# Kernel tuning notes

Measured on AMD Instinct MI355X. Metric: run time of the kernel, lower is better.

The kernel has to match this reference:

```python
import jax, jax.numpy as jnp
import numpy as np

H = 96          # hidden_dim / GatedGraphConv out_channels
L = 6           # num_layers
F_IN = 32       # num_node_features
G = 4096        # number of graphs in batch
BN_EPS = 1e-5


def setup_inputs() -> dict:
    key = jax.random.key(0)
    ks = jax.random.split(key, 16)
    N, E = 100000, 400000
    x = jax.random.normal(ks[0], (N, F_IN), dtype=jnp.float32)
    edge_index = jax.random.randint(ks[1], (2, E), 0, N, dtype=jnp.int64)
    batch = jnp.sort(jax.random.randint(ks[2], (N,), 0, G, dtype=jnp.int64))
    s = 1.0 / np.sqrt(H)
    conv_w = jax.random.uniform(ks[3], (L, H, H), jnp.float32, -s, s)
    w_ih = jax.random.uniform(ks[4], (3 * H, H), jnp.float32, -s, s)
    w_hh = jax.random.uniform(ks[5], (3 * H, H), jnp.float32, -s, s)
    b_ih = jax.random.uniform(ks[6], (3 * H,), jnp.float32, -s, s)
    b_hh = jax.random.uniform(ks[7], (3 * H,), jnp.float32, -s, s)
    bn_gamma = jnp.ones((H,), jnp.float32)
    bn_beta = jnp.zeros((H,), jnp.float32)
    s1 = 1.0 / np.sqrt(H)
    fc1_w = jax.random.uniform(ks[8], (4 * H, H), jnp.float32, -s1, s1)
    fc1_b = jax.random.uniform(ks[9], (4 * H,), jnp.float32, -s1, s1)
    s2 = 1.0 / np.sqrt(4 * H)
    fc2_w = jax.random.uniform(ks[10], (H, 4 * H), jnp.float32, -s2, s2)
    fc2_b = jax.random.uniform(ks[11], (H,), jnp.float32, -s2, s2)
    fc3_w = jax.random.uniform(ks[12], (1, H), jnp.float32, -s1, s1)
    fc3_b = jax.random.uniform(ks[13], (1,), jnp.float32, -s1, s1)
    return dict(x=x, edge_index=edge_index, batch=batch, conv_w=conv_w,
                w_ih=w_ih, w_hh=w_hh, b_ih=b_ih, b_hh=b_hh,
                bn_gamma=bn_gamma, bn_beta=bn_beta,
                fc1_w=fc1_w, fc1_b=fc1_b, fc2_w=fc2_w, fc2_b=fc2_b,
                fc3_w=fc3_w, fc3_b=fc3_b)


def _gated_graph_conv(x, src, dst, conv_w, w_ih, w_hh, b_ih, b_hh):
    N = x.shape[0]
    # PyG zero-pads input features up to out_channels
    h = jnp.pad(x, ((0, 0), (0, H - x.shape[1])))
    for i in range(L):
        m = h @ conv_w[i]                         # [N, H]
        agg = jnp.zeros((N, H), m.dtype).at[dst].add(m[src])  # scatter-add at targets
        gi = agg @ w_ih.T + b_ih                  # [N, 3H]
        gh = h @ w_hh.T + b_hh                    # [N, 3H]
        i_r, i_z, i_n = jnp.split(gi, 3, axis=-1)
        h_r, h_z, h_n = jnp.split(gh, 3, axis=-1)
        r = jax.nn.sigmoid(i_r + h_r)
        z = jax.nn.sigmoid(i_z + h_z)
        n = jnp.tanh(i_n + r * h_n)
        h = (1.0 - z) * n + z * h
    return h


def reference(x, edge_index, batch, conv_w, w_ih, w_hh, b_ih, b_hh,
              bn_gamma, bn_beta, fc1_w, fc1_b, fc2_w, fc2_b, fc3_w, fc3_b):
    src, dst = edge_index[0], edge_index[1]
    h = _gated_graph_conv(x, src, dst, conv_w, w_ih, w_hh, b_ih, b_hh)
    h = jax.nn.relu(h)
    # global mean pool (dropout is identity in eval)
    sums = jax.ops.segment_sum(h, batch, num_segments=G)          # [G, H]
    counts = jax.ops.segment_sum(jnp.ones((h.shape[0],), h.dtype), batch, num_segments=G)
    pooled = sums / jnp.maximum(counts, 1.0)[:, None]
    # BatchNorm1d in eval mode: running_mean=0, running_var=1
    hbn = (pooled / jnp.sqrt(1.0 + BN_EPS)) * bn_gamma + bn_beta
    h1 = jax.nn.relu(hbn @ fc1_w.T + fc1_b)
    h2 = jax.nn.relu(h1 @ fc2_w.T + fc2_b)
    return h2 @ fc3_w.T + fc3_b                                    # [G, 1]
```

## Files before the change

### kernel.cpp

```cpp
#include <hip/hip_runtime.h>

#define H96 96
#define LAYERS 6
#define BN_EPS 1e-5f
#define SCAN_B 1024

typedef unsigned short u16;
typedef unsigned int u32;
typedef _Float16 f16;
typedef _Float16 h8 __attribute__((ext_vector_type(8)));
typedef float f32x4 __attribute__((ext_vector_type(4)));
typedef u32 u32x3 __attribute__((ext_vector_type(3)));

__device__ __forceinline__ float sigm(float x) { return 1.f / (1.f + __expf(-x)); }
__device__ __forceinline__ float tanh_(float x) { return 2.f / (1.f + __expf(-2.f * x)) - 1.f; }
__device__ __forceinline__ f32x4 splat4(float x) { f32x4 v = {x, x, x, x}; return v; }

struct h2s { f16 x, y; };

__device__ __forceinline__ void upk(u32 v, float& lo, float& hi) {
    union { u32 u; h2s h; } c;
    c.u = v;
    lo = (float)c.h.x;
    hi = (float)c.h.y;
}

__global__ void k_f2h(const float* __restrict__ convw, const float* __restrict__ wih,
                      const float* __restrict__ whh, const float* __restrict__ fc1w,
                      const float* __restrict__ fc2w, f16* __restrict__ dst) {
    int i = blockIdx.x * 256 + threadIdx.x;
    if (i >= 184320) return;
    float v;
    if (i < 55296) v = convw[i];
    else if (i < 82944) v = wih[i - 55296];
    else if (i < 110592) v = whh[i - 82944];
    else if (i < 147456) v = fc1w[i - 110592];
    else v = fc2w[i - 147456];
    dst[i] = (f16)v;
}

__global__ __launch_bounds__(256) void k_wpt(const f16* __restrict__ wih16, const f16* __restrict__ convw16,
                                             f16* __restrict__ wpt) {
    int l = blockIdx.y;
    int lane = threadIdx.x & 63, wave = threadIdx.x >> 6;
    int l15 = lane & 15, q = lane >> 4;
    int rowa = blockIdx.x * 64 + wave * 16 + l15;
    if (rowa >= 288) rowa = 287;
    const f16* B = convw16 + (size_t)l * 9216;
    h8 af[3];
#pragma unroll
    for (int s = 0; s < 3; s++) af[s] = *(const h8*)(wih16 + (size_t)rowa * 96 + s * 32 + q * 8);
    f32x4 acc[6];
#pragma unroll
    for (int t = 0; t < 6; t++) acc[t] = splat4(0.f);
#pragma unroll
    for (int s = 0; s < 3; s++)
#pragma unroll
        for (int t = 0; t < 6; t++) {
            h8 b = *(const h8*)(B + (size_t)(t * 16 + l15) * 96 + s * 32 + q * 8);
            acc[t] = __builtin_amdgcn_mfma_f32_16x16x32_f16(af[s], b, acc[t], 0, 0, 0);
        }
    int rbase = blockIdx.x * 64 + wave * 16 + q * 4;
#pragma unroll
    for (int t = 0; t < 6; t++)
#pragma unroll
        for (int rr = 0; rr < 4; rr++) {
            int row = rbase + rr;
            if (row < 288) wpt[(size_t)l * 27648 + (size_t)row * 96 + t * 16 + l15] = (f16)acc[t][rr];
        }
}

__global__ void k_pad(const float* __restrict__ x, f16* __restrict__ hf, int N) {
    int i = blockIdx.x * 256 + threadIdx.x;
    if (i >= N * H96) return;
    int n = i / H96, c = i - n * H96;
    float v = (c < 32) ? x[n * 32 + c] : 0.f;
    hf[i] = (f16)v;
}

__global__ void k_hist(const int* __restrict__ key, int* __restrict__ deg, int E) {
    int e = blockIdx.x * 256 + threadIdx.x;
    if (e < E) atomicAdd(&deg[key[e]], 1);
}

__global__ __launch_bounds__(SCAN_B) void k_scan1(const int* __restrict__ deg, int* __restrict__ incl,
                                                  int* __restrict__ bsum, int N) {
    __shared__ int sh[SCAN_B];
    int i = blockIdx.x * SCAN_B + threadIdx.x;
    int v = (i < N) ? deg[i] : 0;
    sh[threadIdx.x] = v;
    __syncthreads();
    for (int off = 1; off < SCAN_B; off <<= 1) {
        int t = (threadIdx.x >= (u32)off) ? sh[threadIdx.x - off] : 0;
        __syncthreads();
        sh[threadIdx.x] += t;
        __syncthreads();
    }
    incl[blockIdx.x * SCAN_B + threadIdx.x] = sh[threadIdx.x];
    if (threadIdx.x == SCAN_B - 1) bsum[blockIdx.x] = sh[threadIdx.x];
}

__global__ void k_scan2(int* __restrict__ bsum, int nb) {
    if (blockIdx.x == 0 && threadIdx.x == 0) {
        int run = 0;
        for (int i = 0; i < nb; i++) { run += bsum[i]; bsum[i] = run; }
    }
}

__global__ void k_scan3(const int* __restrict__ deg, const int* __restrict__ incl, const int* __restrict__ bsum,
                        int* __restrict__ rs, int* __restrict__ cur, int N, int E) {
    int i = blockIdx.x * 256 + threadIdx.x;
    if (i == 0) rs[N] = E;
    if (i < N) {
        int b = i / SCAN_B;
        int off = (b > 0) ? bsum[b - 1] : 0;
        int ex = incl[i] - deg[i] + off;
        rs[i] = ex;
        if (cur) cur[i] = ex;
    }
}

__global__ void k_fill(const int* __restrict__ src, const int* __restrict__ dst, int* __restrict__ cur,
                       int* __restrict__ es, int E) {
    int e = blockIdx.x * 256 + threadIdx.x;
    if (e < E) {
        int p = atomicAdd(&cur[dst[e]], 1);
        es[p] = src[e];
    }
}

__global__ __launch_bounds__(256) void k_gather(const f16* __restrict__ hin, const int* __restrict__ rs,
                                                const int* __restrict__ es, f16* __restrict__ agg, int N) {
    int grp = threadIdx.x >> 4;
    int lane6 = threadIdx.x & 15;
    int node = blockIdx.x * 16 + grp;
    if (node >= N) return;
    int s = rs[node], e = rs[node + 1];
    float a0 = 0, a1 = 0, a2 = 0, a3 = 0, a4 = 0, a5 = 0;
    const char* basep = (const char*)hin;
    int off = lane6 * 12;
    for (int i = s; i < e; i += 4) {
        int j1 = (i + 1 < e) ? i + 1 : i;
        int j2 = (i + 2 < e) ? i + 2 : i;
        int j3 = (i + 3 < e) ? i + 3 : i;
        float m1 = (i + 1 < e) ? 1.f : 0.f;
        float m2 = (i + 2 < e) ? 1.f : 0.f;
        float m3 = (i + 3 < e) ? 1.f : 0.f;
        int sa = es[i], sb = es[j1], sc = es[j2], sd = es[j3];
        u32x3 va = *(const u32x3*)(basep + (size_t)sa * 192 + off);
        u32x3 vb = *(const u32x3*)(basep + (size_t)sb * 192 + off);
        u32x3 vc = *(const u32x3*)(basep + (size_t)sc * 192 + off);
        u32x3 vd = *(const u32x3*)(basep + (size_t)sd * 192 + off);
        float t0, t1;
        upk(va.x, t0, t1); a0 += t0; a1 += t1;
        upk(va.y, t0, t1); a2 += t0; a3 += t1;
        upk(va.z, t0, t1); a4 += t0; a5 += t1;
        upk(vb.x, t0, t1); a0 += t0 * m1; a1 += t1 * m1;
        upk(vb.y, t0, t1); a2 += t0 * m1; a3 += t1 * m1;
        upk(vb.z, t0, t1); a4 += t0 * m1; a5 += t1 * m1;
        upk(vc.x, t0, t1); a0 += t0 * m2; a1 += t1 * m2;
        upk(vc.y, t0, t1); a2 += t0 * m2; a3 += t1 * m2;
        upk(vc.z, t0, t1); a4 += t0 * m2; a5 += t1 * m2;
        upk(vd.x, t0, t1); a0 += t0 * m3; a1 += t1 * m3;
        upk(vd.y, t0, t1); a2 += t0 * m3; a3 += t1 * m3;
        upk(vd.z, t0, t1); a4 += t0 * m3; a5 += t1 * m3;
    }
    f16* dp = agg + (size_t)node * H96 + lane6 * 6;
    h2s p0, p1, p2;
    p0.x = (f16)a0; p0.y = (f16)a1;
    p1.x = (f16)a2; p1.y = (f16)a3;
    p2.x = (f16)a4; p2.y = (f16)a5;
    *(h2s*)(dp + 0) = p0;
    *(h2s*)(dp + 2) = p1;
    *(h2s*)(dp + 4) = p2;
}

__global__ __launch_bounds__(384, 4) void k_gru(const f16* __restrict__ agg, const f16* __restrict__ hin,
                                                f16* __restrict__ hout, const f16* __restrict__ wpt,
                                                const f16* __restrict__ whh, const float* __restrict__ bih,
                                                const float* __restrict__ bhh, int N) {
    int w = threadIdx.x >> 6;
    int lane = threadIdx.x & 63;
    int l15 = lane & 15, q = lane >> 4;
    int jr = w * 16 + l15;
    float b_r = bih[jr] + bhh[jr];
    float b_z = bih[96 + jr] + bhh[96 + jr];
    float b_in = bih[192 + jr];
    float b_hn = bhh[192 + jr];
    h8 wr0[3], wr1[3], wz0[3], wz1[3], wn0[3], wn1[3];
#pragma unroll
    for (int s = 0; s < 3; s++) {
        int ko = s * 32 + q * 8;
        wr0[s] = *(const h8*)(wpt + (size_t)jr * H96 + ko);
        wz0[s] = *(const h8*)(wpt + (size_t)(96 + jr) * H96 + ko);
        wn0[s] = *(const h8*)(wpt + (size_t)(192 + jr) * H96 + ko);
        wr1[s] = *(const h8*)(whh + (size_t)jr * H96 + ko);
        wz1[s] = *(const h8*)(whh + (size_t)(96 + jr) * H96 + ko);
        wn1[s] = *(const h8*)(whh + (size_t)(192 + jr) * H96 + ko);
    }
    int ntiles = (N + 15) >> 4;
    for (int tile = blockIdx.x; tile < ntiles; tile += gridDim.x) {
        int base = tile << 4;
        int rowa = base + l15;
        if (rowa >= N) rowa = N - 1;
        h8 as_[3], ah[3];
#pragma unroll
        for (int s = 0; s < 3; s++) {
            as_[s] = *(const h8*)(agg + (size_t)rowa * H96 + s * 32 + q * 8);
            ah[s] = *(const h8*)(hin + (size_t)rowa * H96 + s * 32 + q * 8);
        }
        f32x4 r = splat4(b_r), z = splat4(b_z), nn = splat4(b_in), hn = splat4(b_hn);
#pragma unroll
        for (int s = 0; s < 3; s++) {
            r = __builtin_amdgcn_mfma_f32_16x16x32_f16(as_[s], wr0[s], r, 0, 0, 0);
            r = __builtin_amdgcn_mfma_f32_16x16x32_f16(ah[s], wr1[s], r, 0, 0, 0);
            z = __builtin_amdgcn_mfma_f32_16x16x32_f16(as_[s], wz0[s], z, 0, 0, 0);
            z = __builtin_amdgcn_mfma_f32_16x16x32_f16(ah[s], wz1[s], z, 0, 0, 0);
            nn = __builtin_amdgcn_mfma_f32_16x16x32_f16(as_[s], wn0[s], nn, 0, 0, 0);
            hn = __builtin_amdgcn_mfma_f32_16x16x32_f16(ah[s], wn1[s], hn, 0, 0, 0);
        }
        int rbase = base + q * 4;
#pragma unroll
        for (int rr = 0; rr < 4; rr++) {
            int row = rbase + rr;
            if (row < N) {
                float rv = sigm(r[rr]);
                float zv = sigm(z[rr]);
                float nv = tanh_(nn[rr] + rv * hn[rr]);
                size_t idx = (size_t)row * H96 + w * 16 + l15;
                float hold = (float)hin[idx];
                float hnew = (1.f - zv) * nv + zv * hold;
                hout[idx] = (f16)hnew;
            }
        }
    }
}

__global__ void k_pool2(const f16* __restrict__ hf, const int* __restrict__ grs,
                        const float* __restrict__ gamma, const float* __restrict__ beta,
                        f16* __restrict__ pooled, int Gn) {
    int g = blockIdx.x;
    int c = threadIdx.x;
    if (g >= Gn || c >= H96) return;
    int s = grs[g], e = grs[g + 1];
    float sum = 0.f;
    for (int n = s; n < e; n++) sum += fmaxf((float)hf[(size_t)n * H96 + c], 0.f);
    float cnt = fmaxf((float)(e - s), 1.f);
    float val = (sum / cnt) * (gamma[c] * rsqrtf(1.f + BN_EPS)) + beta[c];
    pooled[(size_t)g * H96 + c] = (f16)val;
}

template <int KS, int NT, int OUTW, bool RELU>
__global__ __launch_bounds__(256) void k_mlp(const f16* __restrict__ A, const f16* __restrict__ W,
                                             const float* __restrict__ bias, f16* __restrict__ out, int M) {
    int lane = threadIdx.x & 63, wave = threadIdx.x >> 6;
    int l15 = lane & 15, q = lane >> 4;
    int colBase = blockIdx.y * (NT * 16);
    int tile = blockIdx.x;
    int rowa = tile * 64 + wave * 16 + l15;
    if (rowa >= M) rowa = M - 1;
    h8 af[KS];
#pragma unroll
    for (int s = 0; s < KS; s++) af[s] = *(const h8*)(A + (size_t)rowa * (KS * 32) + s * 32 + q * 8);
    f32x4 acc[NT];
#pragma unroll
    for (int t = 0; t < NT; t++) acc[t] = splat4(0.f);
#pragma unroll
    for (int s = 0; s < KS; s++)
#pragma unroll
        for (int t = 0; t < NT; t++) {
            h8 b = *(const h8*)(W + (size_t)(colBase + t * 16 + l15) * (KS * 32) + s * 32 + q * 8);
            acc[t] = __builtin_amdgcn_mfma_f32_16x16x32_f16(af[s], b, acc[t], 0, 0, 0);
        }
    int rbase = tile * 64 + wave * 16 + q * 4;
#pragma unroll
    for (int t = 0; t < NT; t++) {
        float bv = bias[colBase + t * 16 + l15];
#pragma unroll
        for (int rr = 0; rr < 4; rr++) {
            int row = rbase + rr;
            if (row >= M) continue;
            float v = acc[t][rr] + bv;
            if (RELU) v = fmaxf(v, 0.f);
            out[(size_t)row * OUTW + colBase + t * 16 + l15] = (f16)v;
        }
    }
}

__global__ void k_mlp3(const f16* __restrict__ h2, const float* __restrict__ w, const float* __restrict__ b,
                       float* __restrict__ out, int M) {
    int g = blockIdx.x * 256 + threadIdx.x;
    if (g >= M) return;
    float acc = 0.f;
    for (int k = 0; k < H96; k++) acc += (float)h2[(size_t)g * H96 + k] * w[k];
    out[g] = acc + b[0];
}

extern "C" void kernel_launch(void* const* d_in, const int* in_sizes, int n_in, void* d_out, int out_size,
                              void* d_ws, size_t ws_size, hipStream_t stream) {
    const float* x = (const float*)d_in[0];
    const int* ei = (const int*)d_in[1];
    const int* batch = (const int*)d_in[2];
    const float* conv_w = (const float*)d_in[3];
    const float* wih = (const float*)d_in[4];
    const float* whh = (const float*)d_in[5];
    const float* bih = (const float*)d_in[6];
    const float* bhh = (const float*)d_in[7];
    const float* gamma = (const float*)d_in[8];
    const float* beta = (const float*)d_in[9];
    const float* fc1w = (const float*)d_in[10];
    const float* fc1b = (const float*)d_in[11];
    const float* fc2w = (const float*)d_in[12];
    const float* fc2b = (const float*)d_in[13];
    const float* fc3w = (const float*)d_in[14];
    const float* fc3b = (const float*)d_in[15];

    int N = in_sizes[0] / 32;
    int E = in_sizes[1] / 2;
    int Gn = out_size;
    const int* srcp = ei;
    const int* dstp = ei + E;

    char* p = (char*)d_ws;
    auto alloc = [&](size_t bytes) -> char* {
        char* r = p;
        p += (bytes + 255) & ~(size_t)255;
        return r;
    };
    f16* hA = (f16*)alloc((size_t)N * H96 * 2);
    f16* hB = (f16*)alloc((size_t)N * H96 * 2);
    f16* aggf = (f16*)alloc((size_t)N * H96 * 2);
    f16* wf16 = (f16*)alloc((size_t)184320 * 2);
    f16* wpt = (f16*)alloc((size_t)LAYERS * 27648 * 2);
    int nb = (N + SCAN_B - 1) / SCAN_B;
    int* deg = (int*)alloc((size_t)N * 4);
    int* incl = (int*)alloc((size_t)nb * SCAN_B * 4);
    int* bsum = (int*)alloc((size_t)nb * 4);
    int* rs = (int*)alloc((size_t)(N + 1) * 4);
    int* cur = (int*)alloc((size_t)N * 4);
    int* es = (int*)alloc((size_t)E * 4);
    int nb2 = (Gn + SCAN_B - 1) / SCAN_B;
    int* gdeg = (int*)alloc((size_t)Gn * 4);
    int* gincl = (int*)alloc((size_t)nb2 * SCAN_B * 4);
    int* gbsum = (int*)alloc((size_t)nb2 * 4);
    int* grs = (int*)alloc((size_t)(Gn + 1) * 4);
    f16* pooled = (f16*)alloc((size_t)Gn * H96 * 2);
    f16* h1 = (f16*)alloc((size_t)Gn * 384 * 2);
    f16* h2 = (f16*)alloc((size_t)Gn * H96 * 2);

    f16* convw16 = wf16;
    f16* wih16 = wf16 + 55296;
    f16* whh16 = wf16 + 82944;
    f16* fc1w16 = wf16 + 110592;
    f16* fc2w16 = wf16 + 147456;

    hipMemsetAsync(deg, 0, (size_t)N * 4, stream);
    hipMemsetAsync(gdeg, 0, (size_t)Gn * 4, stream);

    k_f2h<<<720, 256, 0, stream>>>(conv_w, wih, whh, fc1w, fc2w, wf16);
    k_wpt<<<dim3(5, 6), 256, 0, stream>>>(wih16, convw16, wpt);
    k_pad<<<(N * H96 + 255) / 256, 256, 0, stream>>>(x, hA, N);
    k_hist<<<(E + 255) / 256, 256, 0, stream>>>(dstp, deg, E);
    k_scan1<<<nb, SCAN_B, 0, stream>>>(deg, incl, bsum, N);
    k_scan2<<<1, 64, 0, stream>>>(bsum, nb);
    k_scan3<<<(N + 255) / 256, 256, 0, stream>>>(deg, incl, bsum, rs, cur, N, E);
    k_fill<<<(E + 255) / 256, 256, 0, stream>>>(srcp, dstp, cur, es, E);
    k_hist<<<(N + 255) / 256, 256, 0, stream>>>(batch, gdeg, N);
    k_scan1<<<nb2, SCAN_B, 0, stream>>>(gdeg, gincl, gbsum, Gn);
    k_scan2<<<1, 64, 0, stream>>>(gbsum, nb2);
    k_scan3<<<(Gn + 255) / 256, 256, 0, stream>>>(gdeg, gincl, gbsum, grs, (int*)nullptr, Gn, N);

    int nt16 = (N + 15) / 16;
    for (int l = 0; l < LAYERS; l++) {
        f16* hin = (l & 1) ? hB : hA;
        f16* hout = (l & 1) ? hA : hB;
        k_gather<<<nt16, 256, 0, stream>>>(hin, rs, es, aggf, N);
        k_gru<<<1280, 384, 0, stream>>>(aggf, hin, hout, wpt + (size_t)l * 27648, whh16, bih, bhh, N);
    }

    k_pool2<<<Gn, 128, 0, stream>>>(hA, grs, gamma, beta, pooled, Gn);
    k_mlp<3, 6, 384, true><<<dim3((Gn + 63) / 64, 4), 256, 0, stream>>>(pooled, fc1w16, fc1b, h1, Gn);
    k_mlp<12, 6, 96, true><<<dim3((Gn + 63) / 64, 1), 256, 0, stream>>>(h1, fc2w16, fc2b, h2, Gn);
    k_mlp3<<<(Gn + 255) / 256, 256, 0, stream>>>(h2, fc3w, fc3b, (float*)d_out, Gn);
}
```

Measured before the change: 558.1 us.

## Stage GRU weights in LDS and split output columns across blockIdx.y

The GRU kernel now copies half of the combined input/hidden weight rows (144 rows each of wpt and whh) into shared memory once per block. It reads the MFMA B operands from LDS inside the tile loop instead of keeping 36 h8 weight registers per lane. Each block's 6 waves form two row streams of three waves, with blockIdx.y choosing which half of the 96 output columns they compute. The grid shrinks from 1280 blocks to 256x2. This frees registers for occupancy, since the 4-waves launch bound is dropped, at the cost of extra LDS traffic per tile and each node row being read by two blocks.

```diff
diff --git a/kernel.cpp b/kernel.cpp
--- a/kernel.cpp
+++ b/kernel.cpp
@@ -175,49 +175,59 @@
     *(h2s*)(dp + 4) = p2;
 }
 
-__global__ __launch_bounds__(384, 4) void k_gru(const f16* __restrict__ agg, const f16* __restrict__ hin,
-                                                f16* __restrict__ hout, const f16* __restrict__ wpt,
-                                                const f16* __restrict__ whh, const float* __restrict__ bih,
-                                                const float* __restrict__ bhh, int N) {
-    int w = threadIdx.x >> 6;
-    int lane = threadIdx.x & 63;
+__global__ __launch_bounds__(384) void k_gru(const f16* __restrict__ agg, const f16* __restrict__ hin,
+                                             f16* __restrict__ hout, const f16* __restrict__ wpt,
+                                             const f16* __restrict__ whh, const float* __restrict__ bih,
+                                             const float* __restrict__ bhh, int N) {
+    __shared__ __align__(16) f16 lwpt[144 * 96];
+    __shared__ __align__(16) f16 lwhh[144 * 96];
+    int ch = blockIdx.y;
+    int tid = threadIdx.x;
+    for (int c = tid; c < 1728; c += 384) {
+        int lr = c / 12, c8 = c - lr * 12;
+        int g = lr / 48, j = lr - g * 48;
+        int grow = g * 96 + ch * 48 + j;
+        *(h8*)&lwpt[lr * 96 + c8 * 8] = *(const h8*)(wpt + (size_t)grow * 96 + c8 * 8);
+        *(h8*)&lwhh[lr * 96 + c8 * 8] = *(const h8*)(whh + (size_t)grow * 96 + c8 * 8);
+    }
+    __syncthreads();
+    int W = tid >> 6, lane = tid & 63;
+    int wl = W % 3, rstream = W / 3;
     int l15 = lane & 15, q = lane >> 4;
-    int jr = w * 16 + l15;
+    int t = ch * 3 + wl;
+    int jr = t * 16 + l15;
     float b_r = bih[jr] + bhh[jr];
     float b_z = bih[96 + jr] + bhh[96 + jr];
     float b_in = bih[192 + jr];
     float b_hn = bhh[192 + jr];
-    h8 wr0[3], wr1[3], wz0[3], wz1[3], wn0[3], wn1[3];
-#pragma unroll
-    for (int s = 0; s < 3; s++) {
-        int ko = s * 32 + q * 8;
-        wr0[s] = *(const h8*)(wpt + (size_t)jr * H96 + ko);
-        wz0[s] = *(const h8*)(wpt + (size_t)(96 + jr) * H96 + ko);
-        wn0[s] = *(const h8*)(wpt + (size_t)(192 + jr) * H96 + ko);
-        wr1[s] = *(const h8*)(whh + (size_t)jr * H96 + ko);
-        wz1[s] = *(const h8*)(whh + (size_t)(96 + jr) * H96 + ko);
-        wn1[s] = *(const h8*)(whh + (size_t)(192 + jr) * H96 + ko);
-    }
+    int lr0 = wl * 16 + l15;
     int ntiles = (N + 15) >> 4;
-    for (int tile = blockIdx.x; tile < ntiles; tile += gridDim.x) {
+    for (int tile = blockIdx.x * 2 + rstream; tile < ntiles; tile += gridDim.x * 2) {
         int base = tile << 4;
-        int rowa = base + l15;
-        if (rowa >= N) rowa = N - 1;
+        int ra = base + l15;
+        if (ra >= N) ra = N - 1;
         h8 as_[3], ah[3];
 #pragma unroll
         for (int s = 0; s < 3; s++) {
-            as_[s] = *(const h8*)(agg + (size_t)rowa * H96 + s * 32 + q * 8);
-            ah[s] = *(const h8*)(hin + (size_t)rowa * H96 + s * 32 + q * 8);
+            as_[s] = *(const h8*)(agg + (size_t)ra * H96 + s * 32 + q * 8);
+            ah[s] = *(const h8*)(hin + (size_t)ra * H96 + s * 32 + q * 8);
         }
         f32x4 r = splat4(b_r), z = splat4(b_z), nn = splat4(b_in), hn = splat4(b_hn);
 #pragma unroll
         for (int s = 0; s < 3; s++) {
-            r = __builtin_amdgcn_mfma_f32_16x16x32_f16(as_[s], wr0[s], r, 0, 0, 0);
-            r = __builtin_amdgcn_mfma_f32_16x16x32_f16(ah[s], wr1[s], r, 0, 0, 0);
-            z = __builtin_amdgcn_mfma_f32_16x16x32_f16(as_[s], wz0[s], z, 0, 0, 0);
-            z = __builtin_amdgcn_mfma_f32_16x16x32_f16(ah[s], wz1[s], z, 0, 0, 0);
-            nn = __builtin_amdgcn_mfma_f32_16x16x32_f16(as_[s], wn0[s], nn, 0, 0, 0);
-            hn = __builtin_amdgcn_mfma_f32_16x16x32_f16(ah[s], wn1[s], hn, 0, 0, 0);
+            int ko = s * 32 + q * 8;
+            h8 wr0 = *(const h8*)&lwpt[(size_t)lr0 * 96 + ko];
+            h8 wr1 = *(const h8*)&lwhh[(size_t)lr0 * 96 + ko];
+            h8 wz0 = *(const h8*)&lwpt[(size_t)(48 + lr0) * 96 + ko];
+            h8 wz1 = *(const h8*)&lwhh[(size_t)(48 + lr0) * 96 + ko];
+            h8 wn0 = *(const h8*)&lwpt[(size_t)(96 + lr0) * 96 + ko];
+            h8 wn1 = *(const h8*)&lwhh[(size_t)(96 + lr0) * 96 + ko];
+            r = __builtin_amdgcn_mfma_f32_16x16x32_f16(as_[s], wr0, r, 0, 0, 0);
+            r = __builtin_amdgcn_mfma_f32_16x16x32_f16(ah[s], wr1, r, 0, 0, 0);
+            z = __builtin_amdgcn_mfma_f32_16x16x32_f16(as_[s], wz0, z, 0, 0, 0);
+            z = __builtin_amdgcn_mfma_f32_16x16x32_f16(ah[s], wz1, z, 0, 0, 0);
+            nn = __builtin_amdgcn_mfma_f32_16x16x32_f16(as_[s], wn0, nn, 0, 0, 0);
+            hn = __builtin_amdgcn_mfma_f32_16x16x32_f16(ah[s], wn1, hn, 0, 0, 0);
         }
         int rbase = base + q * 4;
 #pragma unroll
@@ -227,7 +237,7 @@
                 float rv = sigm(r[rr]);
                 float zv = sigm(z[rr]);
                 float nv = tanh_(nn[rr] + rv * hn[rr]);
-                size_t idx = (size_t)row * H96 + w * 16 + l15;
+                size_t idx = (size_t)row * H96 + t * 16 + l15;
                 float hold = (float)hin[idx];
                 float hnew = (1.f - zv) * nv + zv * hold;
                 hout[idx] = (f16)hnew;
@@ -375,7 +385,7 @@
         f16* hin = (l & 1) ? hB : hA;
         f16* hout = (l & 1) ? hA : hB;
         k_gather<<<nt16, 256, 0, stream>>>(hin, rs, es, aggf, N);
-        k_gru<<<1280, 384, 0, stream>>>(aggf, hin, hout, wpt + (size_t)l * 27648, whh16, bih, bhh, N);
+        k_gru<<<dim3(256, 2), 384, 0, stream>>>(aggf, hin, hout, wpt + (size_t)l * 27648, whh16, bih, bhh, N);
     }
 
     k_pool2<<<Gn, 128, 0, stream>>>(hA, grs, gamma, beta, pooled, Gn);
```

Result: slower. 587.2 us (+5.2%).

## Restructure GRU kernel with LDS-staged concatenated weights and per-wave row tiles

Applied to the files above, without the earlier changes.

Builds a combined per-layer weight matrix [384 x 192] that stacks the input and hidden projections, so each gate is one K=192 product over the concatenated [agg, h] row. The GRU kernel now stages a 32-column slice of that matrix in shared memory, splits the output columns across blockIdx.y (3 chunks), and gives each wave its own 16-row tile instead of splitting columns across waves. This removes the large per-thread weight register set and aims to improve occupancy and tile parallelism. In exchange, each node row's activations are loaded three times (once per column chunk), the zero-padded blocks add wasted MFMA work, and there is an extra preprocessing kernel.

```diff
diff --git a/kernel.cpp b/kernel.cpp
--- a/kernel.cpp
+++ b/kernel.cpp
@@ -68,6 +68,22 @@
             int row = rbase + rr;
             if (row < 288) wpt[(size_t)l * 27648 + (size_t)row * 96 + t * 16 + l15] = (f16)acc[t][rr];
         }
+}
+
+__global__ void k_bmat(const f16* __restrict__ wpt, const f16* __restrict__ whh16, f16* __restrict__ bmat) {
+    int idx = blockIdx.x * 256 + threadIdx.x;
+    if (idx >= LAYERS * 384 * 192) return;
+    int l = idx / (384 * 192);
+    int rem = idx - l * 384 * 192;
+    int row = rem / 192, k = rem - row * 192;
+    int g = row / 96, j = row - g * 96;
+    f16 v = (f16)0.f;
+    if (g == 0) v = (k < 96) ? wpt[(size_t)l * 27648 + (size_t)j * 96 + k] : whh16[(size_t)j * 96 + k - 96];
+    else if (g == 1) v = (k < 96) ? wpt[(size_t)l * 27648 + (size_t)(96 + j) * 96 + k]
+                                  : whh16[(size_t)(96 + j) * 96 + k - 96];
+    else if (g == 2) { if (k < 96) v = wpt[(size_t)l * 27648 + (size_t)(192 + j) * 96 + k]; }
+    else { if (k >= 96) v = whh16[(size_t)(192 + j) * 96 + k - 96]; }
+    bmat[idx] = v;
 }
 
 __global__ void k_pad(const float* __restrict__ x, f16* __restrict__ hf, int N) {
@@ -175,62 +191,82 @@
     *(h2s*)(dp + 4) = p2;
 }
 
-__global__ __launch_bounds__(384, 4) void k_gru(const f16* __restrict__ agg, const f16* __restrict__ hin,
-                                                f16* __restrict__ hout, const f16* __restrict__ wpt,
-                                                const f16* __restrict__ whh, const float* __restrict__ bih,
-                                                const float* __restrict__ bhh, int N) {
-    int w = threadIdx.x >> 6;
-    int lane = threadIdx.x & 63;
+#define BROW_PAD 200
+__global__ __launch_bounds__(512) void k_gru(const f16* __restrict__ agg, const f16* __restrict__ hin,
+                                             f16* __restrict__ hout, const f16* __restrict__ bmat,
+                                             const float* __restrict__ bih, const float* __restrict__ bhh,
+                                             int N) {
+    __shared__ __align__(16) f16 lwB[128 * BROW_PAD];
+    int ch = blockIdx.y;
+    int tid = threadIdx.x;
+    for (int c = tid; c < 128 * 24; c += 512) {
+        int lr = c / 24, c8 = c - lr * 24;
+        int grow = (lr >> 5) * 96 + ch * 32 + (lr & 31);
+        *(h8*)&lwB[lr * BROW_PAD + c8 * 8] = *(const h8*)(bmat + (size_t)grow * 192 + c8 * 8);
+    }
+    __syncthreads();
+    int w = tid >> 6, lane = tid & 63;
     int l15 = lane & 15, q = lane >> 4;
-    int jr = w * 16 + l15;
-    float b_r = bih[jr] + bhh[jr];
-    float b_z = bih[96 + jr] + bhh[96 + jr];
-    float b_in = bih[192 + jr];
-    float b_hn = bhh[192 + jr];
-    h8 wr0[3], wr1[3], wz0[3], wz1[3], wn0[3], wn1[3];
-#pragma unroll
-    for (int s = 0; s < 3; s++) {
-        int ko = s * 32 + q * 8;
-        wr0[s] = *(const h8*)(wpt + (size_t)jr * H96 + ko);
-        wz0[s] = *(const h8*)(wpt + (size_t)(96 + jr) * H96 + ko);
-        wn0[s] = *(const h8*)(wpt + (size_t)(192 + jr) * H96 + ko);
-        wr1[s] = *(const h8*)(whh + (size_t)jr * H96 + ko);
-        wz1[s] = *(const h8*)(whh + (size_t)(96 + jr) * H96 + ko);
-        wn1[s] = *(const h8*)(whh + (size_t)(192 + jr) * H96 + ko);
+    float bR[2], bZ[2], bNI[2], bNH[2];
+#pragma unroll
+    for (int half = 0; half < 2; half++) {
+        int c = ch * 32 + half * 16 + l15;
+        bR[half] = bih[c] + bhh[c];
+        bZ[half] = bih[96 + c] + bhh[96 + c];
+        bNI[half] = bih[192 + c];
+        bNH[half] = bhh[192 + c];
     }
     int ntiles = (N + 15) >> 4;
-    for (int tile = blockIdx.x; tile < ntiles; tile += gridDim.x) {
+    for (int tile = blockIdx.x * 8 + w; tile < ntiles; tile += gridDim.x * 8) {
         int base = tile << 4;
-        int rowa = base + l15;
-        if (rowa >= N) rowa = N - 1;
-        h8 as_[3], ah[3];
+        int ra = base + l15;
+        if (ra >= N) ra = N - 1;
+        h8 af[6];
 #pragma unroll
         for (int s = 0; s < 3; s++) {
-            as_[s] = *(const h8*)(agg + (size_t)rowa * H96 + s * 32 + q * 8);
-            ah[s] = *(const h8*)(hin + (size_t)rowa * H96 + s * 32 + q * 8);
-        }
-        f32x4 r = splat4(b_r), z = splat4(b_z), nn = splat4(b_in), hn = splat4(b_hn);
-#pragma unroll
-        for (int s = 0; s < 3; s++) {
-            r = __builtin_amdgcn_mfma_f32_16x16x32_f16(as_[s], wr0[s], r, 0, 0, 0);
-            r = __builtin_amdgcn_mfma_f32_16x16x32_f16(ah[s], wr1[s], r, 0, 0, 0);
-            z = __builtin_amdgcn_mfma_f32_16x16x32_f16(as_[s], wz0[s], z, 0, 0, 0);
-            z = __builtin_amdgcn_mfma_f32_16x16x32_f16(ah[s], wz1[s], z, 0, 0, 0);
-            nn = __builtin_amdgcn_mfma_f32_16x16x32_f16(as_[s], wn0[s], nn, 0, 0, 0);
-            hn = __builtin_amdgcn_mfma_f32_16x16x32_f16(ah[s], wn1[s], hn, 0, 0, 0);
-        }
-        int rbase = base + q * 4;
-#pragma unroll
-        for (int rr = 0; rr < 4; rr++) {
-            int row = rbase + rr;
-            if (row < N) {
-                float rv = sigm(r[rr]);
-                float zv = sigm(z[rr]);
-                float nv = tanh_(nn[rr] + rv * hn[rr]);
-                size_t idx = (size_t)row * H96 + w * 16 + l15;
-                float hold = (float)hin[idx];
-                float hnew = (1.f - zv) * nv + zv * hold;
-                hout[idx] = (f16)hnew;
+            af[s] = *(const h8*)(agg + (size_t)ra * H96 + s * 32 + q * 8);
+            af[3 + s] = *(const h8*)(hin + (size_t)ra * H96 + s * 32 + q * 8);
+        }
+        f32x4 aR[2], aZ[2], aNI[2], aNH[2];
+#pragma unroll
+        for (int half = 0; half < 2; half++) {
+            aR[half] = splat4(bR[half]);
+            aZ[half] = splat4(bZ[half]);
+            aNI[half] = splat4(bNI[half]);
+            aNH[half] = splat4(bNH[half]);
+        }
+#pragma unroll
+        for (int s = 0; s < 6; s++) {
+            int ko = s * 32 + q * 8;
+#pragma unroll
+            for (int half = 0; half < 2; half++) {
+                int lr = half * 16 + l15;
+                h8 b0 = *(const h8*)&lwB[(0 * 32 + lr) * BROW_PAD + ko];
+                h8 b1 = *(const h8*)&lwB[(1 * 32 + lr) * BROW_PAD + ko];
+                h8 b2 = *(const h8*)&lwB[(2 * 32 + lr) * BROW_PAD + ko];
+                h8 b3 = *(const h8*)&lwB[(3 * 32 + lr) * BROW_PAD + ko];
+                aR[half] = __builtin_amdgcn_mfma_f32_16x16x32_f16(af[s], b0, aR[half], 0, 0, 0);
+                aZ[half] = __builtin_amdgcn_mfma_f32_16x16x32_f16(af[s], b1, aZ[half], 0, 0, 0);
+                aNI[half] = __builtin_amdgcn_mfma_f32_16x16x32_f16(af[s], b2, aNI[half], 0, 0, 0);
+                aNH[half] = __builtin_amdgcn_mfma_f32_16x16x32_f16(af[s], b3, aNH[half], 0, 0, 0);
+            }
+        }
+#pragma unroll
+        for (int half = 0; half < 2; half++) {
+            int c = ch * 32 + half * 16 + l15;
+            int rbase = base + q * 4;
+#pragma unroll
+            for (int rr = 0; rr < 4; rr++) {
+                int row = rbase + rr;
+                if (row < N) {
+                    float rv = sigm(aR[half][rr]);
+                    float zv = sigm(aZ[half][rr]);
+                    float nv = tanh_(aNI[half][rr] + rv * aNH[half][rr]);
+                    size_t idx = (size_t)row * H96 + c;
+                    float hold = (float)hin[idx];
+                    float hnew = (1.f - zv) * nv + zv * hold;
+                    hout[idx] = (f16)hnew;
+                }
             }
         }
     }
@@ -332,6 +368,7 @@
     f16* aggf = (f16*)alloc((size_t)N * H96 * 2);
     f16* wf16 = (f16*)alloc((size_t)184320 * 2);
     f16* wpt = (f16*)alloc((size_t)LAYERS * 27648 * 2);
+    f16* bmat = (f16*)alloc((size_t)LAYERS * 384 * 192 * 2);
     int nb = (N + SCAN_B - 1) / SCAN_B;
     int* deg = (int*)alloc((size_t)N * 4);
     int* incl = (int*)alloc((size_t)nb * SCAN_B * 4);
@@ -359,6 +396,7 @@
 
     k_f2h<<<720, 256, 0, stream>>>(conv_w, wih, whh, fc1w, fc2w, wf16);
     k_wpt<<<dim3(5, 6), 256, 0, stream>>>(wih16, convw16, wpt);
+    k_bmat<<<(LAYERS * 384 * 192 + 255) / 256, 256, 0, stream>>>(wpt, whh16, bmat);
     k_pad<<<(N * H96 + 255) / 256, 256, 0, stream>>>(x, hA, N);
     k_hist<<<(E + 255) / 256, 256, 0, stream>>>(dstp, deg, E);
     k_scan1<<<nb, SCAN_B, 0, stream>>>(deg, incl, bsum, N);
@@ -371,11 +409,12 @@
     k_scan3<<<(Gn + 255) / 256, 256, 0, stream>>>(gdeg, gincl, gbsum, grs, (int*)nullptr, Gn, N);
 
     int nt16 = (N + 15) / 16;
+    int gx = (nt16 + 7) / 8;
     for (int l = 0; l < LAYERS; l++) {
         f16* hin = (l & 1) ? hB : hA;
         f16* hout = (l & 1) ? hA : hB;
         k_gather<<<nt16, 256, 0, stream>>>(hin, rs, es, aggf, N);
-        k_gru<<<1280, 384, 0, stream>>>(aggf, hin, hout, wpt + (size_t)l * 27648, whh16, bih, bhh, N);
+        k_gru<<<dim3(gx, 3), 512, 0, stream>>>(aggf, hin, hout, bmat + (size_t)l * 384 * 192, bih, bhh, N);
     }
 
     k_pool2<<<Gn, 128, 0, stream>>>(hA, grs, gamma, beta, pooled, Gn);
```

Result: slower. 972.6 us (+74.2%).
